# Kernel tuning notes

Measured on AMD Instinct MI355X. Metric: run time of the kernel, lower is better.

Reference implementation:

```python
import jax, jax.numpy as jnp
import numpy as np

B, S, D = 2, 2048, 2048
H = 16
Q_LORA, KV_LORA = 1536, 512
D_NOPE, D_ROPE, D_V = 128, 64, 128
D_QK = D_NOPE + D_ROPE  # 192
EPS = 1e-6


def rmsnorm(x, w):
    return x * jax.lax.rsqrt(jnp.mean(x * x, axis=-1, keepdims=True) + EPS) * w


def apply_rope(x, freqs_cis):
    # x: (B, S, h, D_ROPE); freqs_cis: (S, D_ROPE//2, 2) = (cos, sin)
    # DeepSeek pairs consecutive elements (2i, 2i+1) as complex re/im.
    b, s, h, d = x.shape
    xp = x.reshape(b, s, h, d // 2, 2)
    re, im = xp[..., 0], xp[..., 1]
    cos = freqs_cis[None, :, None, :, 0]
    sin = freqs_cis[None, :, None, :, 1]
    out_re = re * cos - im * sin
    out_im = re * sin + im * cos
    return jnp.stack([out_re, out_im], axis=-1).reshape(b, s, h, d)


def setup_inputs() -> dict:
    key = jax.random.key(0)
    ks = jax.random.split(key, 8)
    sd = 0.02
    x = jax.random.normal(ks[0], (B, S, D), dtype=jnp.float32)
    # RoPE table over the rope head dim
    inv_freq = 1.0 / (10000.0 ** (np.arange(0, D_ROPE, 2, dtype=np.float32) / D_ROPE))
    t = np.arange(S, dtype=np.float32)
    f = np.outer(t, inv_freq)  # (S, 32)
    freqs_cis = jnp.asarray(np.stack([np.cos(f), np.sin(f)], axis=-1), dtype=jnp.float32)
    return {
        "x": x,
        "start_pos": 0,
        "freqs_cis": freqs_cis,
        "wq_a": jax.random.normal(ks[1], (Q_LORA, D), dtype=jnp.float32) * sd,
        "q_norm_w": jnp.ones((Q_LORA,), dtype=jnp.float32),
        "wq_b": jax.random.normal(ks[2], (H * D_QK, Q_LORA), dtype=jnp.float32) * sd,
        "wkv_a": jax.random.normal(ks[3], (KV_LORA + D_ROPE, D), dtype=jnp.float32) * sd,
        "kv_norm_w": jnp.ones((KV_LORA,), dtype=jnp.float32),
        "wkv_b": jax.random.normal(ks[4], (H * (D_NOPE + D_V), KV_LORA), dtype=jnp.float32) * sd,
        "wo": jax.random.normal(ks[5], (D, H * D_V), dtype=jnp.float32) * sd,
    }


def reference(x, start_pos, freqs_cis, wq_a, q_norm_w, wq_b, wkv_a, kv_norm_w, wkv_b, wo):
    bsz, seqlen, _ = x.shape
    softmax_scale = D_QK ** (-0.5)

    # --- queries: low-rank down-proj, RMSNorm, up-proj ---
    q = rmsnorm(x @ wq_a.T, q_norm_w) @ wq_b.T          # (B,S,H*D_QK)
    q = q.reshape(bsz, seqlen, H, D_QK)
    q_nope, q_pe = q[..., :D_NOPE], q[..., D_NOPE:]
    q_pe = apply_rope(q_pe, freqs_cis)
    q = jnp.concatenate([q_nope, q_pe], axis=-1)         # (B,S,H,192)

    # --- keys/values: compressed latent + shared rope key ---
    kv = x @ wkv_a.T                                     # (B,S,KV_LORA+D_ROPE)
    kv_c, k_pe = kv[..., :KV_LORA], kv[..., KV_LORA:]
    k_pe = apply_rope(k_pe[:, :, None, :], freqs_cis)    # (B,S,1,64)
    kvb = rmsnorm(kv_c, kv_norm_w) @ wkv_b.T             # (B,S,H*(D_NOPE+D_V))
    kvb = kvb.reshape(bsz, seqlen, H, D_NOPE + D_V)
    k_nope, v = kvb[..., :D_NOPE], kvb[..., D_NOPE:]
    k = jnp.concatenate([k_nope, jnp.broadcast_to(k_pe, (bsz, seqlen, H, D_ROPE))], axis=-1)

    # --- causal attention (FA2 with attention_mask=None) ---
    scores = jnp.einsum("bqhd,bkhd->bhqk", q, k) * softmax_scale
    causal = jnp.tril(jnp.ones((seqlen, seqlen), dtype=bool))
    scores = jnp.where(causal[None, None], scores, jnp.finfo(scores.dtype).min)
    attn = jax.nn.softmax(scores, axis=-1)
    out = jnp.einsum("bhqk,bkhd->bqhd", attn, v)         # (B,S,H,D_V)
    # (v padding to qk_head_dim then slicing [..., :D_V] is a no-op)
    return out.reshape(bsz, seqlen, H * D_V) @ wo.T
```

## Files before the change

kernel.cpp:

```cpp
#include <hip/hip_runtime.h>
#include <math.h>

typedef short short8 __attribute__((ext_vector_type(8)));
typedef float float4v __attribute__((ext_vector_type(4)));
#define AS1 __attribute__((address_space(1)))
#define AS3 __attribute__((address_space(3)))

__device__ __forceinline__ float b2f(ushort u) {
    unsigned v = ((unsigned)u) << 16; float f; __builtin_memcpy(&f, &v, 4); return f;
}
__device__ __forceinline__ ushort f2b(float f) {
    unsigned v; __builtin_memcpy(&v, &f, 4);
    unsigned r = (v + 0x7fffu + ((v >> 16) & 1u)) >> 16;
    return (ushort)r;
}

__global__ void cvt_pad(const float* __restrict__ src, ushort* __restrict__ dst,
                        int src_rows, int cols, int total4, float scl) {
    int i = blockIdx.x * 256 + threadIdx.x;
    if (i >= total4) return;
    size_t e = (size_t)i * 4;
    int r = (int)(e / (size_t)cols);
    ushort4 o;
    if (r < src_rows) {
        float4 v = *(const float4*)(src + e);
        o.x = f2b(v.x * scl); o.y = f2b(v.y * scl); o.z = f2b(v.z * scl); o.w = f2b(v.w * scl);
    } else {
        o.x = 0; o.y = 0; o.z = 0; o.w = 0;
    }
    *(ushort4*)(dst + e) = o;
}

__global__ __launch_bounds__(256)
void gemm_bt(const ushort* __restrict__ A, const ushort* __restrict__ B,
             void* __restrict__ Cv, int K, int lda, int ldb, int ldc, int mode,
             ushort* __restrict__ Kf, ushort* __restrict__ Vtp) {
    __shared__ ushort sA[128 * 32];
    __shared__ ushort sB[128 * 32];
    const int tid = threadIdx.x;
    const int wave = tid >> 6, lane = tid & 63;
    const int bm = blockIdx.y * 128, bn = blockIdx.x * 128;
    const int wm = (wave >> 1) * 64, wn = (wave & 1) * 64;
    const int lq = lane & 15, quad = lane >> 4;
    float4v acc[4][4] = {};

    const int srow = wave * 32 + (lane >> 2);
    const int skc = (lane & 3) * 8;
    const ushort* Ag = A + (size_t)(bm + srow) * lda + skc;
    const ushort* Bg = B + (size_t)(bn + srow) * ldb + skc;
    ushort* sAw = sA + (wave * 32) * 32;
    ushort* sBw = sB + (wave * 32) * 32;

    for (int k0 = 0; k0 < K; k0 += 32) {
        __builtin_amdgcn_global_load_lds((const AS1 void*)(Ag + k0), (AS3 void*)sAw, 16, 0, 0);
        __builtin_amdgcn_global_load_lds((const AS1 void*)(Ag + (size_t)16 * lda + k0),
                                         (AS3 void*)(sAw + 16 * 32), 16, 0, 0);
        __builtin_amdgcn_global_load_lds((const AS1 void*)(Bg + k0), (AS3 void*)sBw, 16, 0, 0);
        __builtin_amdgcn_global_load_lds((const AS1 void*)(Bg + (size_t)16 * ldb + k0),
                                         (AS3 void*)(sBw + 16 * 32), 16, 0, 0);
        __syncthreads();
        short8 af[4], bfr[4];
#pragma unroll
        for (int i = 0; i < 4; ++i) {
            af[i]  = *(const short8*)(sA + (wm + i * 16 + lq) * 32 + quad * 8);
            bfr[i] = *(const short8*)(sB + (wn + i * 16 + lq) * 32 + quad * 8);
        }
#pragma unroll
        for (int i = 0; i < 4; ++i)
#pragma unroll
            for (int j = 0; j < 4; ++j)
                acc[i][j] = __builtin_amdgcn_mfma_f32_16x16x32_bf16(af[i], bfr[j], acc[i][j], 0, 0, 0);
        __syncthreads();
    }
#pragma unroll
    for (int i = 0; i < 4; ++i) {
        int row0 = bm + wm + i * 16 + quad * 4;
#pragma unroll
        for (int j = 0; j < 4; ++j) {
            int col = bn + wn + j * 16 + lq;
            if (mode == 0) {
                ushort* C = (ushort*)Cv;
#pragma unroll
                for (int r = 0; r < 4; ++r)
                    C[(size_t)(row0 + r) * ldc + col] = f2b(acc[i][j][r]);
            } else if (mode == 1) {
                float* C = (float*)Cv;
#pragma unroll
                for (int r = 0; r < 4; ++r)
                    C[(size_t)(row0 + r) * ldc + col] = acc[i][j][r];
            } else {
                int h = col >> 8, c = col & 255;
                int bh = ((row0 >> 11) << 4) + h;
                if (c < 128) {
#pragma unroll
                    for (int r = 0; r < 4; ++r) {
                        int s = (row0 + r) & 2047;
                        Kf[((size_t)bh * 2048 + s) * 200 + c] = f2b(acc[i][j][r]);
                    }
                } else {
                    int d = c - 128;
                    int kt = (row0 & 2047) >> 6, kv = row0 & 63;
                    ushort4 o;
                    o.x = f2b(acc[i][j][0]); o.y = f2b(acc[i][j][1]);
                    o.z = f2b(acc[i][j][2]); o.w = f2b(acc[i][j][3]);
                    *(ushort4*)(Vtp + (((size_t)bh * 32 + kt) * 128 + d) * 72 + kv) = o;
                }
            }
        }
    }
}

__global__ void rmsnorm_inplace(ushort* __restrict__ d, const float* __restrict__ w,
                                int cols, int ld) {
    int row = blockIdx.x, tid = threadIdx.x;
    ushort* p = d + (size_t)row * ld;
    float ss = 0.f;
    for (int i = tid; i < cols; i += 256) { float v = b2f(p[i]); ss += v * v; }
#pragma unroll
    for (int off = 32; off >= 1; off >>= 1) ss += __shfl_xor(ss, off);
    __shared__ float red[4];
    if ((tid & 63) == 0) red[tid >> 6] = ss;
    __syncthreads();
    float tot = red[0] + red[1] + red[2] + red[3];
    float rs = rsqrtf(tot / (float)cols + 1e-6f);
    for (int i = tid; i < cols; i += 256) p[i] = f2b(b2f(p[i]) * rs * w[i]);
}

__global__ void kvnorm_rope(const ushort* __restrict__ kvraw, const float* __restrict__ w,
                            const float* __restrict__ freqs, ushort* __restrict__ kvc,
                            ushort* __restrict__ kpe, int ld) {
    int row = blockIdx.x, tid = threadIdx.x;
    int s = row & 2047;
    const ushort* p = kvraw + (size_t)row * ld;
    float v0 = b2f(p[tid]), v1 = b2f(p[tid + 256]);
    float ss = v0 * v0 + v1 * v1;
#pragma unroll
    for (int off = 32; off >= 1; off >>= 1) ss += __shfl_xor(ss, off);
    __shared__ float red[4];
    if ((tid & 63) == 0) red[tid >> 6] = ss;
    __syncthreads();
    float tot = red[0] + red[1] + red[2] + red[3];
    float rs = rsqrtf(tot / 512.f + 1e-6f);
    kvc[(size_t)row * 512 + tid] = f2b(v0 * rs * w[tid]);
    kvc[(size_t)row * 512 + tid + 256] = f2b(v1 * rs * w[tid + 256]);
    if (tid < 32) {
        float re = b2f(p[512 + 2 * tid]), im = b2f(p[512 + 2 * tid + 1]);
        float cs = freqs[(s * 32 + tid) * 2], sn = freqs[(s * 32 + tid) * 2 + 1];
        kpe[(size_t)row * 64 + 2 * tid] = f2b(re * cs - im * sn);
        kpe[(size_t)row * 64 + 2 * tid + 1] = f2b(re * sn + im * cs);
    }
}

__global__ void qrope(ushort* __restrict__ q, const float* __restrict__ freqs) {
    int idx = blockIdx.x * 256 + threadIdx.x;
    int i = idx & 31;
    int h = (idx >> 5) & 15;
    int srow = idx >> 9;
    int s = srow & 2047;
    ushort* p = q + ((size_t)srow * 16 + h) * 192 + 128 + 2 * i;
    float re = b2f(p[0]), im = b2f(p[1]);
    float cs = freqs[(s * 32 + i) * 2], sn = freqs[(s * 32 + i) * 2 + 1];
    p[0] = f2b(re * cs - im * sn);
    p[1] = f2b(re * sn + im * cs);
}

__global__ void kpe_fill(const ushort* __restrict__ kpe, ushort* __restrict__ Kfull) {
    int tid = threadIdx.x;
    int row = blockIdx.x * 8 + (tid >> 5);
    int c = tid & 31;
    int bh = row >> 11, s = row & 2047, b = bh >> 4;
    ushort2 v;
    v.x = kpe[((size_t)b * 2048 + s) * 64 + 2 * c];
    v.y = kpe[((size_t)b * 2048 + s) * 64 + 2 * c + 1];
    *(ushort2*)(Kfull + (size_t)row * 200 + 128 + 2 * c) = v;
}

__global__ __launch_bounds__(256, 3)
void mla_attn7(const ushort* __restrict__ q, const ushort* __restrict__ Kfull,
               const ushort* __restrict__ Vt, ushort* __restrict__ out) {
    __shared__ ushort sK[64 * 200];
    __shared__ ushort sV[128 * 72];
    __shared__ ushort sP[4][16][72];
    const int tid = threadIdx.x, wave = tid >> 6, lane = tid & 63;
    const int lq = lane & 15, quad = lane >> 4;
    const int lin = blockIdx.x;
    const int e = lin & 7, idx = lin >> 3;
    const int qt = 31 - (idx >> 2);
    const int bh = e + 8 * (idx & 3);
    const int b = bh >> 4, h = bh & 15;
    const ushort* Kb = Kfull + (size_t)bh * 2048 * 200;
    const ushort* Vb = Vt + (size_t)bh * 32 * 128 * 72;
    const int slot = wave * 64 + lane;

    const int qrow = qt * 64 + wave * 16 + lq;
    const ushort* qp = q + ((size_t)(b * 2048 + qrow) * 16 + h) * 192 + quad * 8;
    short8 qf[6];
#pragma unroll
    for (int c = 0; c < 6; ++c) qf[c] = *(const short8*)(qp + c * 32);

    short8 kreg[7], vreg[5];
#pragma unroll
    for (int i = 0; i < 7; ++i) {
        int s0 = i * 256 + slot;
        if (s0 < 1600) kreg[i] = *(const short8*)(Kb + (size_t)s0 * 8);
    }
#pragma unroll
    for (int i = 0; i < 5; ++i) {
        int s0 = i * 256 + slot;
        if (s0 < 1152) vreg[i] = *(const short8*)(Vb + (size_t)s0 * 8);
    }

    float4v oacc[8] = {};
    float m_i[4] = {-INFINITY, -INFINITY, -INFINITY, -INFINITY};
    float l_i[4] = {0.f, 0.f, 0.f, 0.f};
    const int myrow0 = qt * 64 + wave * 16 + quad * 4;

    for (int kt = 0; kt <= qt; ++kt) {
#pragma unroll
        for (int i = 0; i < 7; ++i) {
            int s0 = i * 256 + slot;
            if (s0 < 1600) *(short8*)(sK + (size_t)s0 * 8) = kreg[i];
        }
#pragma unroll
        for (int i = 0; i < 5; ++i) {
            int s0 = i * 256 + slot;
            if (s0 < 1152) *(short8*)(sV + (size_t)s0 * 8) = vreg[i];
        }
        __syncthreads();
        if (kt < qt) {
            const ushort* Ksrc = Kb + (size_t)(kt + 1) * 64 * 200;
            const ushort* Vsrc = Vb + (size_t)(kt + 1) * 128 * 72;
#pragma unroll
            for (int i = 0; i < 7; ++i) {
                int s0 = i * 256 + slot;
                if (s0 < 1600) kreg[i] = *(const short8*)(Ksrc + (size_t)s0 * 8);
            }
#pragma unroll
            for (int i = 0; i < 5; ++i) {
                int s0 = i * 256 + slot;
                if (s0 < 1152) vreg[i] = *(const short8*)(Vsrc + (size_t)s0 * 8);
            }
        }
        float4v sc[4];
#pragma unroll
        for (int ct = 0; ct < 4; ++ct) {
            float4v a = {0.f, 0.f, 0.f, 0.f};
#pragma unroll
            for (int c = 0; c < 6; ++c) {
                short8 kf = *(const short8*)(sK + (ct * 16 + lq) * 200 + c * 32 + quad * 8);
                a = __builtin_amdgcn_mfma_f32_16x16x32_bf16(qf[c], kf, a, 0, 0, 0);
            }
            sc[ct] = a;
        }
        float mnew[4];
#pragma unroll
        for (int r = 0; r < 4; ++r) mnew[r] = m_i[r];
#pragma unroll
        for (int ct = 0; ct < 4; ++ct)
#pragma unroll
            for (int r = 0; r < 4; ++r) {
                float v = sc[ct][r];
                if (kt == qt && (kt * 64 + ct * 16 + lq) > (myrow0 + r)) v = -INFINITY;
                sc[ct][r] = v;
                mnew[r] = fmaxf(mnew[r], v);
            }
#pragma unroll
        for (int off = 8; off >= 1; off >>= 1)
#pragma unroll
            for (int r = 0; r < 4; ++r) mnew[r] = fmaxf(mnew[r], __shfl_xor(mnew[r], off));
        float g = mnew[0] - m_i[0];
#pragma unroll
        for (int r = 1; r < 4; ++r) g = fmaxf(g, mnew[r] - m_i[r]);
        if (__ballot(g > 8.0f) != 0ull) {
#pragma unroll
            for (int r = 0; r < 4; ++r) {
                float a = __builtin_amdgcn_exp2f(m_i[r] - mnew[r]);
                m_i[r] = mnew[r];
                l_i[r] *= a;
#pragma unroll
                for (int dt = 0; dt < 8; ++dt) oacc[dt][r] *= a;
            }
        }
        float psum[4] = {0.f, 0.f, 0.f, 0.f};
#pragma unroll
        for (int ct = 0; ct < 4; ++ct)
#pragma unroll
            for (int r = 0; r < 4; ++r) {
                float pv = __builtin_amdgcn_exp2f(sc[ct][r] - m_i[r]);
                psum[r] += pv;
                sP[wave][quad * 4 + r][ct * 16 + lq] = f2b(pv);
            }
#pragma unroll
        for (int off = 8; off >= 1; off >>= 1)
#pragma unroll
            for (int r = 0; r < 4; ++r) psum[r] += __shfl_xor(psum[r], off);
#pragma unroll
        for (int r = 0; r < 4; ++r) l_i[r] += psum[r];
#pragma unroll
        for (int kc = 0; kc < 2; ++kc) {
            short8 pf = *(const short8*)(&sP[wave][lq][kc * 32 + quad * 8]);
#pragma unroll
            for (int dt = 0; dt < 8; ++dt) {
                short8 vf = *(const short8*)(sV + (dt * 16 + lq) * 72 + kc * 32 + quad * 8);
                oacc[dt] = __builtin_amdgcn_mfma_f32_16x16x32_bf16(pf, vf, oacc[dt], 0, 0, 0);
            }
        }
        __syncthreads();
    }
    float inv[4];
#pragma unroll
    for (int r = 0; r < 4; ++r) inv[r] = 1.f / l_i[r];
#pragma unroll
    for (int dt = 0; dt < 8; ++dt) {
#pragma unroll
        for (int r = 0; r < 4; ++r) {
            out[((size_t)(b * 2048 + myrow0 + r) * 16 + h) * 128 + dt * 16 + lq] =
                f2b(oacc[dt][r] * inv[r]);
        }
    }
}

extern "C" void kernel_launch(void* const* d_in, const int* in_sizes, int n_in,
                              void* d_out, int out_size, void* d_ws, size_t ws_size,
                              hipStream_t stream) {
    const float* x     = (const float*)d_in[0];
    const float* freqs = (const float*)d_in[2];
    const float* wq_a  = (const float*)d_in[3];
    const float* qnw   = (const float*)d_in[4];
    const float* wq_b  = (const float*)d_in[5];
    const float* wkv_a = (const float*)d_in[6];
    const float* kvnw  = (const float*)d_in[7];
    const float* wkv_b = (const float*)d_in[8];
    const float* wo    = (const float*)d_in[9];

    char* ws = (char*)d_ws;
    size_t off = 0;
    auto alloc = [&](size_t n) { char* p = ws + off; off += (n + 255) & ~(size_t)255; return p; };
    ushort* xb    = (ushort*)alloc(4096ull * 2048 * 2);
    ushort* wqkva = (ushort*)alloc(2176ull * 2048 * 2);
    ushort* wqbb  = (ushort*)alloc(3072ull * 1536 * 2);
    ushort* wkvbb = (ushort*)alloc(4096ull * 512 * 2);
    ushort* wob   = (ushort*)alloc(2048ull * 2048 * 2);
    ushort* qakv  = (ushort*)alloc(4096ull * 2176 * 2);
    ushort* kvc   = (ushort*)alloc(4096ull * 512 * 2);
    ushort* kpe   = (ushort*)alloc(4096ull * 64 * 2);
    ushort* qfull = (ushort*)alloc(4096ull * 3072 * 2);
    ushort* kvbuf = (ushort*)alloc(4096ull * 4096 * 2);
    ushort* attno = (ushort*)alloc(4096ull * 2048 * 2);
    if (off > ws_size) return;
    ushort* Kfull = kvbuf;
    ushort* Vt = xb;

    auto cvt = [&](const float* s, ushort* dd, int sr, int cols, size_t dtot, float scl) {
        int t4 = (int)(dtot / 4);
        cvt_pad<<<(t4 + 255) / 256, 256, 0, stream>>>(s, dd, sr, cols, t4, scl);
    };
    const float qk_scale = 1.44269504f / sqrtf(192.0f);
    cvt(x, xb, 4096, 2048, 4096ull * 2048, 1.f);
    cvt(wq_a, wqkva, 1536, 2048, 1536ull * 2048, 1.f);
    cvt(wkv_a, wqkva + 1536ull * 2048, 576, 2048, 640ull * 2048, 1.f);
    cvt(wq_b, wqbb, 3072, 1536, 3072ull * 1536, qk_scale);
    cvt(wkv_b, wkvbb, 4096, 512, 4096ull * 512, 1.f);
    cvt(wo, wob, 2048, 2048, 2048ull * 2048, 1.f);

    gemm_bt<<<dim3(17, 32), 256, 0, stream>>>(xb, wqkva, qakv, 2048, 2048, 2048, 2176, 0, nullptr, nullptr);
    rmsnorm_inplace<<<4096, 256, 0, stream>>>(qakv, qnw, 1536, 2176);
    kvnorm_rope<<<4096, 256, 0, stream>>>(qakv + 1536, kvnw, freqs, kvc, kpe, 2176);
    gemm_bt<<<dim3(24, 32), 256, 0, stream>>>(qakv, wqbb, qfull, 1536, 2176, 1536, 3072, 0, nullptr, nullptr);
    qrope<<<8192, 256, 0, stream>>>(qfull, freqs);
    kpe_fill<<<8192, 256, 0, stream>>>(kpe, Kfull);
    gemm_bt<<<dim3(32, 32), 256, 0, stream>>>(kvc, wkvbb, nullptr, 512, 512, 512, 0, 2, Kfull, Vt);
    mla_attn7<<<dim3(1024), 256, 0, stream>>>(qfull, Kfull, Vt, attno);
    gemm_bt<<<dim3(16, 32), 256, 0, stream>>>(attno, wob, (float*)d_out, 2048, 2048, 2048, 2048, 1, nullptr, nullptr);
}
```

Measured before the change: 509.7 us.

## Load K/V fragments directly from global memory instead of staging through LDS

The attention kernel no longer stages K and V tiles into shared memory with a register prefetch and block barriers. Each wave now reads its MFMA operand fragments for K and V straight from global memory, relying on L2/L1 caching since all four waves read the same tiles. This removes the LDS stores, the LDS reads and both __syncthreads per tile, and frees LDS for occupancy. In exchange it gives up explicit prefetch overlap and quadruples global/cache traffic, so latency may be exposed.

```diff
diff --git a/kernel.cpp b/kernel.cpp
--- a/kernel.cpp
+++ b/kernel.cpp
@@ -176,10 +176,8 @@
 }
 
 __global__ __launch_bounds__(256, 3)
-void mla_attn7(const ushort* __restrict__ q, const ushort* __restrict__ Kfull,
+void mla_attn8(const ushort* __restrict__ q, const ushort* __restrict__ Kfull,
                const ushort* __restrict__ Vt, ushort* __restrict__ out) {
-    __shared__ ushort sK[64 * 200];
-    __shared__ ushort sV[128 * 72];
     __shared__ ushort sP[4][16][72];
     const int tid = threadIdx.x, wave = tid >> 6, lane = tid & 63;
     const int lq = lane & 15, quad = lane >> 4;
@@ -190,25 +188,12 @@
     const int b = bh >> 4, h = bh & 15;
     const ushort* Kb = Kfull + (size_t)bh * 2048 * 200;
     const ushort* Vb = Vt + (size_t)bh * 32 * 128 * 72;
-    const int slot = wave * 64 + lane;
 
     const int qrow = qt * 64 + wave * 16 + lq;
     const ushort* qp = q + ((size_t)(b * 2048 + qrow) * 16 + h) * 192 + quad * 8;
     short8 qf[6];
 #pragma unroll
     for (int c = 0; c < 6; ++c) qf[c] = *(const short8*)(qp + c * 32);
-
-    short8 kreg[7], vreg[5];
-#pragma unroll
-    for (int i = 0; i < 7; ++i) {
-        int s0 = i * 256 + slot;
-        if (s0 < 1600) kreg[i] = *(const short8*)(Kb + (size_t)s0 * 8);
-    }
-#pragma unroll
-    for (int i = 0; i < 5; ++i) {
-        int s0 = i * 256 + slot;
-        if (s0 < 1152) vreg[i] = *(const short8*)(Vb + (size_t)s0 * 8);
-    }
 
     float4v oacc[8] = {};
     float m_i[4] = {-INFINITY, -INFINITY, -INFINITY, -INFINITY};
@@ -216,42 +201,25 @@
     const int myrow0 = qt * 64 + wave * 16 + quad * 4;
 
     for (int kt = 0; kt <= qt; ++kt) {
-#pragma unroll
-        for (int i = 0; i < 7; ++i) {
-            int s0 = i * 256 + slot;
-            if (s0 < 1600) *(short8*)(sK + (size_t)s0 * 8) = kreg[i];
-        }
-#pragma unroll
-        for (int i = 0; i < 5; ++i) {
-            int s0 = i * 256 + slot;
-            if (s0 < 1152) *(short8*)(sV + (size_t)s0 * 8) = vreg[i];
-        }
-        __syncthreads();
-        if (kt < qt) {
-            const ushort* Ksrc = Kb + (size_t)(kt + 1) * 64 * 200;
-            const ushort* Vsrc = Vb + (size_t)(kt + 1) * 128 * 72;
-#pragma unroll
-            for (int i = 0; i < 7; ++i) {
-                int s0 = i * 256 + slot;
-                if (s0 < 1600) kreg[i] = *(const short8*)(Ksrc + (size_t)s0 * 8);
-            }
-#pragma unroll
-            for (int i = 0; i < 5; ++i) {
-                int s0 = i * 256 + slot;
-                if (s0 < 1152) vreg[i] = *(const short8*)(Vsrc + (size_t)s0 * 8);
-            }
-        }
+        const ushort* Krow = Kb + (size_t)(kt * 64 + lq) * 200 + quad * 8;
+        const ushort* Vrow = Vb + (size_t)kt * 128 * 72 + (size_t)lq * 72 + quad * 8;
         float4v sc[4];
 #pragma unroll
         for (int ct = 0; ct < 4; ++ct) {
+            short8 kf[6];
+#pragma unroll
+            for (int c = 0; c < 6; ++c)
+                kf[c] = *(const short8*)(Krow + (size_t)ct * 16 * 200 + c * 32);
             float4v a = {0.f, 0.f, 0.f, 0.f};
 #pragma unroll
-            for (int c = 0; c < 6; ++c) {
-                short8 kf = *(const short8*)(sK + (ct * 16 + lq) * 200 + c * 32 + quad * 8);
-                a = __builtin_amdgcn_mfma_f32_16x16x32_bf16(qf[c], kf, a, 0, 0, 0);
-            }
+            for (int c = 0; c < 6; ++c)
+                a = __builtin_amdgcn_mfma_f32_16x16x32_bf16(qf[c], kf[c], a, 0, 0, 0);
             sc[ct] = a;
         }
+        short8 vf0[8];
+#pragma unroll
+        for (int dt = 0; dt < 8; ++dt)
+            vf0[dt] = *(const short8*)(Vrow + (size_t)dt * 16 * 72);
         float mnew[4];
 #pragma unroll
         for (int r = 0; r < 4; ++r) mnew[r] = m_i[r];
@@ -301,11 +269,11 @@
             short8 pf = *(const short8*)(&sP[wave][lq][kc * 32 + quad * 8]);
 #pragma unroll
             for (int dt = 0; dt < 8; ++dt) {
-                short8 vf = *(const short8*)(sV + (dt * 16 + lq) * 72 + kc * 32 + quad * 8);
+                short8 vf = kc == 0 ? vf0[dt]
+                                    : *(const short8*)(Vrow + (size_t)dt * 16 * 72 + 32);
                 oacc[dt] = __builtin_amdgcn_mfma_f32_16x16x32_bf16(pf, vf, oacc[dt], 0, 0, 0);
             }
         }
-        __syncthreads();
     }
     float inv[4];
 #pragma unroll
@@ -370,6 +338,6 @@
     qrope<<<8192, 256, 0, stream>>>(qfull, freqs);
     kpe_fill<<<8192, 256, 0, stream>>>(kpe, Kfull);
     gemm_bt<<<dim3(32, 32), 256, 0, stream>>>(kvc, wkvbb, nullptr, 512, 512, 512, 0, 2, Kfull, Vt);
-    mla_attn7<<<dim3(1024), 256, 0, stream>>>(qfull, Kfull, Vt, attno);
+    mla_attn8<<<dim3(1024), 256, 0, stream>>>(qfull, Kfull, Vt, attno);
     gemm_bt<<<dim3(16, 32), 256, 0, stream>>>(attno, wob, (float*)d_out, 2048, 2048, 2048, 2048, 1, nullptr, nullptr);
 }
```

After: 569.6 us. 11.8% more time.
